# Performance work log

Measured on AMD Instinct MI355X. Metric: run time of the kernel, lower is better.

Reference implementation:

```python
import jax, jax.numpy as jnp
import numpy as np

B, N_PATCH, N_TABLE, N_CLS, E, H = 2, 2048, 16, 1, 512, 8
N = N_PATCH + N_TABLE + N_CLS  # 2065
D = E // H
SCALE = D ** -0.5
EPS = 1e-6


def setup_inputs() -> dict:
    key = jax.random.key(0)
    k0, k1, k2 = jax.random.split(key, 3)
    # 0.02 weight scale keeps A_raw moderate so the module's un-shifted exp() is stable,
    # matching typical trained-weight magnitudes.
    x = jax.random.normal(k0, (B, N, E), jnp.float32)
    w_qkv = jax.random.normal(k1, (E, 3 * E), jnp.float32) * 0.02
    b_qkv = jnp.zeros((3 * E,), jnp.float32)
    w_out = jax.random.normal(k2, (E, E), jnp.float32) * 0.02
    b_out = jnp.zeros((E,), jnp.float32)
    return {"x": x, "w_qkv": w_qkv, "b_qkv": b_qkv, "w_out": w_out, "b_out": b_out}


def _balanced_attention(A_raw):
    # Segmented softmax: patch / table / cls each normalized separately (no max-shift,
    # +1e-6 in denominator — faithful to the torch source), then mixed by a 3-way
    # softmax over (patch-mean, table-mean, cls-max) segment statistics.
    Ap = A_raw[..., :N_PATCH]
    At = A_raw[..., N_PATCH:N_PATCH + N_TABLE]
    Ac = A_raw[..., N_PATCH + N_TABLE:]
    ep = jnp.exp(Ap.mean(-1, keepdims=True))
    et = jnp.exp(At.mean(-1, keepdims=True))
    ec = jnp.exp(Ac.max(-1, keepdims=True))
    s = ep + et + ec
    def seg(a, w):
        e = jnp.exp(a)
        return e / (e.sum(-1, keepdims=True) + EPS) * w
    return jnp.concatenate([seg(Ap, ep / s), seg(At, et / s), seg(Ac, ec / s)], axis=-1)


def reference(x, w_qkv, b_qkv, w_out, b_out):
    qkv = x @ w_qkv + b_qkv                       # [B, N, 3E]
    q, k, v = jnp.split(qkv, 3, axis=-1)
    to_heads = lambda t: t.reshape(B, N, H, D).transpose(0, 2, 1, 3)  # b n (h d) -> b h n d
    q, k, v = to_heads(q), to_heads(k), to_heads(v)
    A_raw = jnp.einsum('bhnd,bhmd->bhnm', q, k) * SCALE
    A = _balanced_attention(A_raw)
    # dropout is identity in eval mode
    out = jnp.einsum('bhnm,bhmd->bhnd', A, v)
    out = out.transpose(0, 2, 1, 3).reshape(B, N, E)  # b h n d -> b n (h d)
    out = out @ w_out + b_out
    return (out, A, A_raw)
```

## Files before the change

### kernel.cpp

```cpp
#include <hip/hip_runtime.h>
#include <hip/hip_bf16.h>

#define BB     2
#define NN     2065
#define NPAD   2112
#define HH     8
#define DD     64
#define EE     512
#define MROWS  (BB*NN)
#define NPATCH 2048
#define NTAB   16
#define SCALEF 0.125f
#define EPSF   1e-6f

typedef __bf16 bf16;
typedef bf16  bf16x8 __attribute__((ext_vector_type(8)));
typedef bf16  bf16x4v __attribute__((ext_vector_type(4)));
typedef float f32x4  __attribute__((ext_vector_type(4)));

#define LDS_STRIDE 72

__global__ __launch_bounds__(256) void k_zero(uint4* __restrict__ p, int n4) {
    int i = blockIdx.x * 256 + threadIdx.x;
    if (i < n4) { uint4 z = {0,0,0,0}; p[i] = z; }
}

__global__ __launch_bounds__(256) void k_cvt(const float* __restrict__ x,
                                             bf16* __restrict__ o, int n4) {
    int i = blockIdx.x * 256 + threadIdx.x;
    if (i < n4) {
        float4 v = ((const float4*)x)[i];
        bf16x4v r;
        r[0] = (bf16)v.x; r[1] = (bf16)v.y; r[2] = (bf16)v.z; r[3] = (bf16)v.w;
        *(bf16x4v*)(o + 4*(size_t)i) = r;
    }
}

__global__ __launch_bounds__(256) void k_transcvt(const float* __restrict__ w,
                                                  bf16* __restrict__ o,
                                                  int C, int total) {
    int i = blockIdx.x * 256 + threadIdx.x;
    if (i < total) {
        int k = i & 511, c = i >> 9;
        o[i] = (bf16)w[(size_t)k * C + c];
    }
}

__global__ __launch_bounds__(256) void k_gemm_qkv(
    const bf16* __restrict__ xb, const bf16* __restrict__ wt,
    const float* __restrict__ bias,
    bf16* __restrict__ Qh, bf16* __restrict__ Kh, bf16* __restrict__ Vt)
{
    __shared__ bf16 As[64][LDS_STRIDE];
    __shared__ bf16 Bs[64][LDS_STRIDE];
    int t = threadIdx.x;
    int w = t >> 6, l = t & 63, l15 = l & 15, quad = l >> 4;
    int m0 = blockIdx.y * 64, c0 = blockIdx.x * 64;
    int srow = t >> 2, sseg = (t & 3) * 16;
    f32x4 acc[4] = {};

    for (int kk = 0; kk < 512; kk += 64) {
        {
            int m = m0 + srow;
            uint4 v0 = {0,0,0,0}, v1 = {0,0,0,0};
            if (m < MROWS) {
                const uint4* src = (const uint4*)(xb + (size_t)m*512 + kk + sseg);
                v0 = src[0]; v1 = src[1];
            }
            *(uint4*)&As[srow][sseg]     = v0;
            *(uint4*)&As[srow][sseg + 8] = v1;
            const uint4* bs = (const uint4*)(wt + (size_t)(c0 + srow)*512 + kk + sseg);
            *(uint4*)&Bs[srow][sseg]     = bs[0];
            *(uint4*)&Bs[srow][sseg + 8] = bs[1];
        }
        __syncthreads();
        #pragma unroll
        for (int kh = 0; kh < 2; kh++) {
            bf16x8 a = *(const bf16x8*)&As[w*16 + l15][kh*32 + quad*8];
            #pragma unroll
            for (int c = 0; c < 4; c++) {
                bf16x8 b = *(const bf16x8*)&Bs[c*16 + l15][kh*32 + quad*8];
                acc[c] = __builtin_amdgcn_mfma_f32_16x16x32_bf16(a, b, acc[c], 0, 0, 0);
            }
        }
        __syncthreads();
    }

    int which = c0 >> 9;
    int h = (c0 & 511) >> 6;
    #pragma unroll
    for (int c = 0; c < 4; c++) {
        int d  = (c0 & 63) + c*16 + l15;
        float bv = bias[c0 + c*16 + l15];
        #pragma unroll
        for (int r = 0; r < 4; r++) {
            int m = m0 + w*16 + quad*4 + r;
            if (m >= MROWS) continue;
            int b_ = m / NN, n = m - b_ * NN;
            int bh = b_ * 8 + h;
            float v = acc[c][r] + bv;
            if (which == 0)      Qh[(size_t)(bh*NPAD + n)*64 + d] = (bf16)v;
            else if (which == 1) Kh[(size_t)(bh*NPAD + n)*64 + d] = (bf16)v;
            else                 Vt[((size_t)bh*64 + d)*NPAD + n] = (bf16)v;
        }
    }
}

__global__ __launch_bounds__(256) void k_attn1(
    const bf16* __restrict__ Qh, const bf16* __restrict__ Kh,
    float* __restrict__ Araw, float4* __restrict__ stats)
{
    __shared__ bf16 Qs[64][LDS_STRIDE];
    __shared__ bf16 Ks[64][LDS_STRIDE];
    int t = threadIdx.x;
    int w = t >> 6, l = t & 63, l15 = l & 15, quad = l >> 4;
    int n0 = blockIdx.x * 64;
    int bh = blockIdx.y;
    int srow = t >> 2, sseg = (t & 3) * 16;
    {
        const uint4* src = (const uint4*)(Qh + (size_t)(bh*NPAD + n0 + srow)*64 + sseg);
        *(uint4*)&Qs[srow][sseg]     = src[0];
        *(uint4*)&Qs[srow][sseg + 8] = src[1];
    }
    float sp[4]  = {0,0,0,0}, sep[4] = {0,0,0,0};
    float st[4]  = {0,0,0,0}, set_[4] = {0,0,0,0}, cv[4] = {0,0,0,0};
    int nrow[4];
    #pragma unroll
    for (int r = 0; r < 4; r++) nrow[r] = n0 + w*16 + quad*4 + r;

    for (int kt = 0; kt < 33; kt++) {
        __syncthreads();
        {
            const uint4* src = (const uint4*)(Kh + (size_t)(bh*NPAD + kt*64 + srow)*64 + sseg);
            *(uint4*)&Ks[srow][sseg]     = src[0];
            *(uint4*)&Ks[srow][sseg + 8] = src[1];
        }
        __syncthreads();
        f32x4 acc[4] = {};
        #pragma unroll
        for (int kh = 0; kh < 2; kh++) {
            bf16x8 a = *(const bf16x8*)&Qs[w*16 + l15][kh*32 + quad*8];
            #pragma unroll
            for (int c = 0; c < 4; c++) {
                bf16x8 b = *(const bf16x8*)&Ks[c*16 + l15][kh*32 + quad*8];
                acc[c] = __builtin_amdgcn_mfma_f32_16x16x32_bf16(a, b, acc[c], 0, 0, 0);
            }
        }
        #pragma unroll
        for (int c = 0; c < 4; c++) {
            int col = kt*64 + c*16 + l15;
            #pragma unroll
            for (int r = 0; r < 4; r++) {
                float val = acc[c][r] * SCALEF;
                float e = __expf(val);
                if (col < NPATCH)            { sp[r] += val; sep[r] += e; }
                else if (col < NPATCH+NTAB)  { st[r] += val; set_[r] += e; }
                else if (col == NPATCH+NTAB) { cv[r] = val; }
                if (col < NN && nrow[r] < NN)
                    Araw[((size_t)(bh*NN + nrow[r]))*NN + col] = val;
            }
        }
    }
    #pragma unroll
    for (int r = 0; r < 4; r++) {
        #pragma unroll
        for (int m = 1; m < 16; m <<= 1) {
            sp[r]   += __shfl_xor(sp[r],   m, 64);
            sep[r]  += __shfl_xor(sep[r],  m, 64);
            st[r]   += __shfl_xor(st[r],   m, 64);
            set_[r] += __shfl_xor(set_[r], m, 64);
            cv[r]   += __shfl_xor(cv[r],   m, 64);
        }
    }
    if (l15 == 0) {
        #pragma unroll
        for (int r = 0; r < 4; r++) {
            if (nrow[r] < NN) {
                float ep = __expf(sp[r] * (1.0f / NPATCH));
                float et = __expf(st[r] * (1.0f / NTAB));
                float ec = __expf(cv[r]);
                float s  = ep + et + ec;
                float4 o;
                o.x = ep / (s * (sep[r]  + EPSF));
                o.y = et / (s * (set_[r] + EPSF));
                o.z = ec / (s * (ec      + EPSF));
                o.w = 0.f;
                stats[bh*NPAD + nrow[r]] = o;
            }
        }
    }
}

__global__ __launch_bounds__(256) void k_attn2(
    const bf16* __restrict__ Qh, const bf16* __restrict__ Kh,
    const bf16* __restrict__ Vt, const float4* __restrict__ stats,
    float* __restrict__ A, bf16* __restrict__ attn)
{
    __shared__ bf16 Qs[64][LDS_STRIDE];
    __shared__ bf16 Ks[64][LDS_STRIDE];
    __shared__ bf16 Vs[64][LDS_STRIDE];
    __shared__ bf16 Ps[64][LDS_STRIDE];
    int t = threadIdx.x;
    int w = t >> 6, l = t & 63, l15 = l & 15, quad = l >> 4;
    int n0 = blockIdx.x * 64;
    int bh = blockIdx.y;
    int srow = t >> 2, sseg = (t & 3) * 16;
    {
        const uint4* src = (const uint4*)(Qh + (size_t)(bh*NPAD + n0 + srow)*64 + sseg);
        *(uint4*)&Qs[srow][sseg]     = src[0];
        *(uint4*)&Qs[srow][sseg + 8] = src[1];
    }
    int nrow[4];
    float cp[4], ctb[4], cc[4];
    #pragma unroll
    for (int r = 0; r < 4; r++) {
        nrow[r] = n0 + w*16 + quad*4 + r;
        float4 s4 = stats[bh*NPAD + nrow[r]];
        cp[r] = s4.x; ctb[r] = s4.y; cc[r] = s4.z;
    }
    f32x4 o[4] = {};

    for (int kt = 0; kt < 33; kt++) {
        __syncthreads();
        {
            const uint4* ks = (const uint4*)(Kh + (size_t)(bh*NPAD + kt*64 + srow)*64 + sseg);
            *(uint4*)&Ks[srow][sseg]     = ks[0];
            *(uint4*)&Ks[srow][sseg + 8] = ks[1];
            const uint4* vs = (const uint4*)(Vt + ((size_t)bh*64 + srow)*NPAD + kt*64 + sseg);
            *(uint4*)&Vs[srow][sseg]     = vs[0];
            *(uint4*)&Vs[srow][sseg + 8] = vs[1];
        }
        __syncthreads();
        f32x4 acc[4] = {};
        #pragma unroll
        for (int kh = 0; kh < 2; kh++) {
            bf16x8 a = *(const bf16x8*)&Qs[w*16 + l15][kh*32 + quad*8];
            #pragma unroll
            for (int c = 0; c < 4; c++) {
                bf16x8 b = *(const bf16x8*)&Ks[c*16 + l15][kh*32 + quad*8];
                acc[c] = __builtin_amdgcn_mfma_f32_16x16x32_bf16(a, b, acc[c], 0, 0, 0);
            }
        }
        #pragma unroll
        for (int c = 0; c < 4; c++) {
            int col = kt*64 + c*16 + l15;
            #pragma unroll
            for (int r = 0; r < 4; r++) {
                float val = acc[c][r] * SCALEF;
                float e = __expf(val);
                float coef = (col < NPATCH) ? cp[r]
                           : (col < NPATCH+NTAB) ? ctb[r]
                           : (col == NPATCH+NTAB) ? cc[r] : 0.f;
                float av = e * coef;
                if (col < NN && nrow[r] < NN)
                    A[((size_t)(bh*NN + nrow[r]))*NN + col] = av;
                Ps[w*16 + quad*4 + r][c*16 + l15] = (bf16)av;
            }
        }
        __syncthreads();
        #pragma unroll
        for (int kh = 0; kh < 2; kh++) {
            bf16x8 pa = *(const bf16x8*)&Ps[w*16 + l15][kh*32 + quad*8];
            #pragma unroll
            for (int g = 0; g < 4; g++) {
                bf16x8 vb = *(const bf16x8*)&Vs[g*16 + l15][kh*32 + quad*8];
                o[g] = __builtin_amdgcn_mfma_f32_16x16x32_bf16(pa, vb, o[g], 0, 0, 0);
            }
        }
    }
    int b_ = bh >> 3, h = bh & 7;
    #pragma unroll
    for (int g = 0; g < 4; g++) {
        #pragma unroll
        for (int r = 0; r < 4; r++) {
            int n = nrow[r];
            if (n < NN)
                attn[((size_t)(b_*NN + n))*512 + h*64 + g*16 + l15] = (bf16)o[g][r];
        }
    }
}

__global__ __launch_bounds__(256) void k_gemm_out(
    const bf16* __restrict__ attn, const bf16* __restrict__ wt,
    const float* __restrict__ bias, float* __restrict__ out)
{
    __shared__ bf16 As[64][LDS_STRIDE];
    __shared__ bf16 Bs[64][LDS_STRIDE];
    int t = threadIdx.x;
    int w = t >> 6, l = t & 63, l15 = l & 15, quad = l >> 4;
    int m0 = blockIdx.y * 64, c0 = blockIdx.x * 64;
    int srow = t >> 2, sseg = (t & 3) * 16;
    f32x4 acc[4] = {};

    for (int kk = 0; kk < 512; kk += 64) {
        {
            int m = m0 + srow;
            uint4 v0 = {0,0,0,0}, v1 = {0,0,0,0};
            if (m < MROWS) {
                const uint4* src = (const uint4*)(attn + (size_t)m*512 + kk + sseg);
                v0 = src[0]; v1 = src[1];
            }
            *(uint4*)&As[srow][sseg]     = v0;
            *(uint4*)&As[srow][sseg + 8] = v1;
            const uint4* bs = (const uint4*)(wt + (size_t)(c0 + srow)*512 + kk + sseg);
            *(uint4*)&Bs[srow][sseg]     = bs[0];
            *(uint4*)&Bs[srow][sseg + 8] = bs[1];
        }
        __syncthreads();
        #pragma unroll
        for (int kh = 0; kh < 2; kh++) {
            bf16x8 a = *(const bf16x8*)&As[w*16 + l15][kh*32 + quad*8];
            #pragma unroll
            for (int c = 0; c < 4; c++) {
                bf16x8 b = *(const bf16x8*)&Bs[c*16 + l15][kh*32 + quad*8];
                acc[c] = __builtin_amdgcn_mfma_f32_16x16x32_bf16(a, b, acc[c], 0, 0, 0);
            }
        }
        __syncthreads();
    }
    #pragma unroll
    for (int c = 0; c < 4; c++) {
        int col = c0 + c*16 + l15;
        float bv = bias[col];
        #pragma unroll
        for (int r = 0; r < 4; r++) {
            int m = m0 + w*16 + quad*4 + r;
            if (m < MROWS)
                out[(size_t)m*512 + col] = acc[c][r] + bv;
        }
    }
}

extern "C" void kernel_launch(void* const* d_in, const int* in_sizes, int n_in,
                              void* d_out, int out_size, void* d_ws, size_t ws_size,
                              hipStream_t stream)
{
    const float* x     = (const float*)d_in[0];
    const float* w_qkv = (const float*)d_in[1];
    const float* b_qkv = (const float*)d_in[2];
    const float* w_out = (const float*)d_in[3];
    const float* b_out = (const float*)d_in[4];

    float* out  = (float*)d_out;
    float* A    = out + (size_t)MROWS * 512;
    float* Araw = A   + (size_t)BB * HH * NN * NN;

    char* ws = (char*)d_ws;
    size_t off = 0;
    auto alloc = [&](size_t bytes) {
        char* p = ws + off;
        off += (bytes + 255) & ~(size_t)255;
        return p;
    };
    bf16*  xb    = (bf16*)alloc((size_t)MROWS * 512 * 2);
    bf16*  wqt   = (bf16*)alloc((size_t)1536 * 512 * 2);
    bf16*  wot   = (bf16*)alloc((size_t)512 * 512 * 2);
    bf16*  Qh    = (bf16*)alloc((size_t)16 * NPAD * 64 * 2);
    bf16*  Kh    = (bf16*)alloc((size_t)16 * NPAD * 64 * 2);
    bf16*  Vt    = (bf16*)alloc((size_t)16 * NPAD * 64 * 2);
    float4* stats = (float4*)alloc((size_t)16 * NPAD * 16);
    bf16*  attn  = (bf16*)alloc((size_t)MROWS * 512 * 2);
    (void)ws_size; (void)in_sizes; (void)n_in; (void)out_size;

    int zero4 = (int)((size_t)3 * 16 * NPAD * 64 * 2 / 16);
    k_zero<<<dim3((zero4 + 255) / 256), 256, 0, stream>>>((uint4*)Qh, zero4);

    k_cvt<<<dim3((MROWS*512/4 + 255) / 256), 256, 0, stream>>>(x, xb, MROWS*512/4);
    k_transcvt<<<dim3(1536*512/256), 256, 0, stream>>>(w_qkv, wqt, 1536, 1536*512);
    k_transcvt<<<dim3(512*512/256),  256, 0, stream>>>(w_out, wot, 512,  512*512);

    k_gemm_qkv<<<dim3(24, 65), 256, 0, stream>>>(xb, wqt, b_qkv, Qh, Kh, Vt);
    k_attn1<<<dim3(33, 16), 256, 0, stream>>>(Qh, Kh, Araw, stats);
    k_attn2<<<dim3(33, 16), 256, 0, stream>>>(Qh, Kh, Vt, stats, A, attn);
    k_gemm_out<<<dim3(8, 65), 256, 0, stream>>>(attn, wot, b_out, out);
}
```

Baseline: 729.7 us.

## Double-buffer K tiles and halve row tile in first attention pass

The first attention kernel now processes 32 query rows per block instead of 64, launching twice as many blocks. The four waves split the key tile into two column halves. K tiles are double-buffered through registers and LDS, so each iteration needs one barrier instead of two. Q fragments are hoisted into registers, and the per-row statistics from the two column halves are combined through shared memory. The aim is more parallelism and overlap of K loads with MFMA work, at the cost of reading K twice as often in total.

Measured after the change: 744.5 us. 1.02x slower.

```diff
diff --git a/kernel.cpp b/kernel.cpp
--- a/kernel.cpp
+++ b/kernel.cpp
@@ -110,59 +110,90 @@
     const bf16* __restrict__ Qh, const bf16* __restrict__ Kh,
     float* __restrict__ Araw, float4* __restrict__ stats)
 {
-    __shared__ bf16 Qs[64][LDS_STRIDE];
-    __shared__ bf16 Ks[64][LDS_STRIDE];
+    __shared__ bf16 Qs[32][LDS_STRIDE];
+    __shared__ bf16 Ks[2][64][LDS_STRIDE];
+    __shared__ float sRed[2][32][6];
+
     int t = threadIdx.x;
     int w = t >> 6, l = t & 63, l15 = l & 15, quad = l >> 4;
-    int n0 = blockIdx.x * 64;
+    int n0 = blockIdx.x * 32;
     int bh = blockIdx.y;
-    int srow = t >> 2, sseg = (t & 3) * 16;
+    int r0 = (w & 1) * 16;
+    int ch = (w >> 1);
+
     {
-        const uint4* src = (const uint4*)(Qh + (size_t)(bh*NPAD + n0 + srow)*64 + sseg);
-        *(uint4*)&Qs[srow][sseg]     = src[0];
-        *(uint4*)&Qs[srow][sseg + 8] = src[1];
-    }
-    float sp[4]  = {0,0,0,0}, sep[4] = {0,0,0,0};
+        int qrow = t >> 3, qseg = (t & 7) * 8;
+        *(uint4*)&Qs[qrow][qseg] =
+            *(const uint4*)(Qh + ((size_t)bh*NPAD + n0 + qrow)*64 + qseg);
+    }
+
+    int krow = t >> 2, kseg = (t & 3) * 16;
+    const bf16* kbase = Kh + ((size_t)bh*NPAD)*64 + (size_t)krow*64 + kseg;
+    uint4 kv0, kv1;
+
+    {
+        const uint4* s = (const uint4*)(kbase);
+        kv0 = s[0]; kv1 = s[1];
+        *(uint4*)&Ks[0][krow][kseg]     = kv0;
+        *(uint4*)&Ks[0][krow][kseg + 8] = kv1;
+        const uint4* s1 = (const uint4*)(kbase + (size_t)64*64);
+        kv0 = s1[0]; kv1 = s1[1];
+    }
+    __syncthreads();
+
+    bf16x8 qa0 = *(const bf16x8*)&Qs[r0 + l15][quad*8];
+    bf16x8 qa1 = *(const bf16x8*)&Qs[r0 + l15][32 + quad*8];
+
+    int nrow[4]; bool vr[4]; size_t rbase[4];
+    #pragma unroll
+    for (int r = 0; r < 4; ++r) {
+        nrow[r] = n0 + quad*4 + r;
+        nrow[r] += r0;
+        vr[r] = nrow[r] < NN;
+        rbase[r] = ((size_t)(bh*NN) + nrow[r]) * NN;
+    }
+
+    float sp[4]  = {0,0,0,0}, sep[4]  = {0,0,0,0};
     float st[4]  = {0,0,0,0}, set_[4] = {0,0,0,0}, cv[4] = {0,0,0,0};
-    int nrow[4];
-    #pragma unroll
-    for (int r = 0; r < 4; r++) nrow[r] = n0 + w*16 + quad*4 + r;
-
-    for (int kt = 0; kt < 33; kt++) {
-        __syncthreads();
-        {
-            const uint4* src = (const uint4*)(Kh + (size_t)(bh*NPAD + kt*64 + srow)*64 + sseg);
-            *(uint4*)&Ks[srow][sseg]     = src[0];
-            *(uint4*)&Ks[srow][sseg + 8] = src[1];
-        }
-        __syncthreads();
-        f32x4 acc[4] = {};
-        #pragma unroll
-        for (int kh = 0; kh < 2; kh++) {
-            bf16x8 a = *(const bf16x8*)&Qs[w*16 + l15][kh*32 + quad*8];
-            #pragma unroll
-            for (int c = 0; c < 4; c++) {
-                bf16x8 b = *(const bf16x8*)&Ks[c*16 + l15][kh*32 + quad*8];
-                acc[c] = __builtin_amdgcn_mfma_f32_16x16x32_bf16(a, b, acc[c], 0, 0, 0);
-            }
-        }
-        #pragma unroll
-        for (int c = 0; c < 4; c++) {
-            int col = kt*64 + c*16 + l15;
-            #pragma unroll
-            for (int r = 0; r < 4; r++) {
+
+    for (int kt = 0; kt < 33; ++kt) {
+        int cur = kt & 1;
+        f32x4 acc[2] = {};
+        #pragma unroll
+        for (int c = 0; c < 2; ++c) {
+            bf16x8 b0 = *(const bf16x8*)&Ks[cur][ch*32 + c*16 + l15][quad*8];
+            bf16x8 b1 = *(const bf16x8*)&Ks[cur][ch*32 + c*16 + l15][32 + quad*8];
+            acc[c] = __builtin_amdgcn_mfma_f32_16x16x32_bf16(qa0, b0, acc[c], 0, 0, 0);
+            acc[c] = __builtin_amdgcn_mfma_f32_16x16x32_bf16(qa1, b1, acc[c], 0, 0, 0);
+        }
+        #pragma unroll
+        for (int c = 0; c < 2; ++c) {
+            int col = kt*64 + ch*32 + c*16 + l15;
+            bool colNN = col < NN;
+            #pragma unroll
+            for (int r = 0; r < 4; ++r) {
                 float val = acc[c][r] * SCALEF;
                 float e = __expf(val);
                 if (col < NPATCH)            { sp[r] += val; sep[r] += e; }
                 else if (col < NPATCH+NTAB)  { st[r] += val; set_[r] += e; }
                 else if (col == NPATCH+NTAB) { cv[r] = val; }
-                if (col < NN && nrow[r] < NN)
-                    Araw[((size_t)(bh*NN + nrow[r]))*NN + col] = val;
-            }
-        }
-    }
-    #pragma unroll
-    for (int r = 0; r < 4; r++) {
+                if (colNN && vr[r])
+                    Araw[rbase[r] + col] = val;
+            }
+        }
+        if (kt < 32) {
+            *(uint4*)&Ks[cur ^ 1][krow][kseg]     = kv0;
+            *(uint4*)&Ks[cur ^ 1][krow][kseg + 8] = kv1;
+        }
+        if (kt < 31) {
+            const uint4* s = (const uint4*)(kbase + (size_t)(kt + 2)*64*64);
+            kv0 = s[0]; kv1 = s[1];
+        }
+        __syncthreads();
+    }
+
+    #pragma unroll
+    for (int r = 0; r < 4; ++r) {
         #pragma unroll
         for (int m = 1; m < 16; m <<= 1) {
             sp[r]   += __shfl_xor(sp[r],   m, 64);
@@ -174,19 +205,34 @@
     }
     if (l15 == 0) {
         #pragma unroll
-        for (int r = 0; r < 4; r++) {
-            if (nrow[r] < NN) {
-                float ep = __expf(sp[r] * (1.0f / NPATCH));
-                float et = __expf(st[r] * (1.0f / NTAB));
-                float ec = __expf(cv[r]);
-                float s  = ep + et + ec;
-                float4 o;
-                o.x = ep / (s * (sep[r]  + EPSF));
-                o.y = et / (s * (set_[r] + EPSF));
-                o.z = ec / (s * (ec      + EPSF));
-                o.w = 0.f;
-                stats[bh*NPAD + nrow[r]] = o;
-            }
+        for (int r = 0; r < 4; ++r) {
+            int row = r0 + quad*4 + r;
+            sRed[ch][row][0] = sp[r];
+            sRed[ch][row][1] = sep[r];
+            sRed[ch][row][2] = st[r];
+            sRed[ch][row][3] = set_[r];
+            sRed[ch][row][4] = cv[r];
+        }
+    }
+    __syncthreads();
+    if (t < 32) {
+        int n = n0 + t;
+        if (n < NN) {
+            float spt  = sRed[0][t][0] + sRed[1][t][0];
+            float sept = sRed[0][t][1] + sRed[1][t][1];
+            float stt  = sRed[0][t][2] + sRed[1][t][2];
+            float sett = sRed[0][t][3] + sRed[1][t][3];
+            float cvt_ = sRed[0][t][4] + sRed[1][t][4];
+            float ep = __expf(spt * (1.0f / NPATCH));
+            float et = __expf(stt * (1.0f / NTAB));
+            float ec = __expf(cvt_);
+            float s  = ep + et + ec;
+            float4 o;
+            o.x = ep / (s * (sept + EPSF));
+            o.y = et / (s * (sett + EPSF));
+            o.z = ec / (s * (ec   + EPSF));
+            o.w = 0.f;
+            stats[bh*NPAD + n] = o;
         }
     }
 }
@@ -370,7 +416,7 @@
     k_transcvt<<<dim3(512*512/256),  256, 0, stream>>>(w_out, wot, 512,  512*512);
 
     k_gemm_qkv<<<dim3(24, 65), 256, 0, stream>>>(xb, wqt, b_qkv, Qh, Kh, Vt);
-    k_attn1<<<dim3(33, 16), 256, 0, stream>>>(Qh, Kh, Araw, stats);
+    k_attn1<<<dim3(66, 16), 256, 0, stream>>>(Qh, Kh, Araw, stats);
     k_attn2<<<dim3(33, 16), 256, 0, stream>>>(Qh, Kh, Vt, stats, A, attn);
     k_gemm_out<<<dim3(8, 65), 256, 0, stream>>>(attn, wot, b_out, out);
 }
```
